# Optimization experiments

Hardware: AMD Instinct MI355X
Metric: run time of the kernel (lower is better)

Reference implementation:

```python
import jax, jax.numpy as jnp
import numpy as np

B, C, H, W = 8, 512, 32, 32
N_HEADS, HEAD_DIM = 8, 64
EPS = 1e-5


def _layernorm(x, g, b):
    mu = jnp.mean(x, axis=-1, keepdims=True)
    var = jnp.mean(jnp.square(x - mu), axis=-1, keepdims=True)
    return (x - mu) * jax.lax.rsqrt(var + EPS) * g + b


def setup_inputs() -> dict:
    key = jax.random.key(0)
    ks = jax.random.split(key, 16)
    u = lambda k, shp: jax.random.uniform(k, shp, dtype=jnp.float32)
    inp = {
        "x": jax.random.normal(ks[0], (B, C, H, W), dtype=jnp.float32),
        "t": jax.random.normal(ks[1], (B,), dtype=jnp.float32),
        # attention params (torch.rand init in source)
        "K_W": u(ks[2], (N_HEADS, C, HEAD_DIM)), "K_b": u(ks[3], (N_HEADS, HEAD_DIM)),
        "Q_W": u(ks[4], (N_HEADS, C, HEAD_DIM)), "Q_b": u(ks[5], (N_HEADS, HEAD_DIM)),
        "V_W": u(ks[6], (N_HEADS, C, HEAD_DIM)), "V_b": u(ks[7], (N_HEADS, HEAD_DIM)),
        "O_W": u(ks[8], (N_HEADS, HEAD_DIM, C)), "O_b": u(ks[9], (C,)),
        # pre-attention LayerNorm
        "ln1_g": jnp.ones((C,), jnp.float32), "ln1_b": jnp.zeros((C,), jnp.float32),
        # MLP: LayerNorm -> Linear -> GELU -> Linear
        "ln2_g": jnp.ones((C,), jnp.float32), "ln2_b": jnp.zeros((C,), jnp.float32),
        "W1": jax.random.normal(ks[10], (C, C), dtype=jnp.float32) / np.sqrt(C),
        "b1": jnp.zeros((C,), jnp.float32),
        "W2": jax.random.normal(ks[11], (C, C), dtype=jnp.float32) / np.sqrt(C),
        "b2": jnp.zeros((C,), jnp.float32),
    }
    return inp


def reference(x, t, K_W, K_b, Q_W, Q_b, V_W, V_b, O_W, O_b,
              ln1_g, ln1_b, ln2_g, ln2_b, W1, b1, W2, b2):
    b, c, h, w = x.shape
    xs = x.reshape(b, c, h * w).transpose(0, 2, 1)           # b s c
    res = _layernorm(xs, ln1_g, ln1_b)
    q = jnp.einsum('bsc,ncd->bsnd', res, Q_W) + Q_b          # b s n_h h_dim
    k = jnp.einsum('bsc,ncd->bsnd', res, K_W) + K_b
    v = jnp.einsum('bsc,ncd->bsnd', res, V_W) + V_b
    scores = jnp.einsum('bsnd,btnd->bnst', q, k) / jnp.sqrt(jnp.float32(c))
    attn = jax.nn.softmax(scores, axis=-1)                   # b n_h s s
    o = jnp.einsum('bnst,btnd->bsnd', attn, v)
    out = jnp.einsum('bsnd,ndc->bsc', o, O_W) + O_b
    out = out + xs                                           # residual
    m = _layernorm(out, ln2_g, ln2_b)
    m = jax.nn.gelu(m @ W1 + b1, approximate=False) @ W2 + b2
    out = m + out
    return out.transpose(0, 2, 1).reshape(b, c, h, w)
```

## Files before the change

### kernel.cpp

```cpp
#include <hip/hip_runtime.h>
#include <math.h>

#define BB 8
#define CC 512
#define SS 1024
#define NHH 8
#define HDD 64
#define KD 512

typedef __attribute__((ext_vector_type(8))) short short8;
typedef __attribute__((ext_vector_type(4))) float f32x4;
typedef __attribute__((ext_vector_type(4))) unsigned short ushort4v;
typedef __attribute__((ext_vector_type(8))) unsigned short ushort8v;
typedef __attribute__((ext_vector_type(2))) unsigned int u32x2;

__device__ __forceinline__ unsigned short f2bf(float x) {
  union { float f; unsigned int u; } c; c.f = x;
  unsigned int r = (c.u + 0x7FFFu + ((c.u >> 16) & 1u)) >> 16;
  return (unsigned short)r;
}
__device__ __forceinline__ float b2f(unsigned short h) {
  union { unsigned int u; float f; } c; c.u = ((unsigned int)h) << 16; return c.f;
}

#define GLD_LDS(gp, lp) __builtin_amdgcn_global_load_lds( \
    (const __attribute__((address_space(1))) void*)(gp),  \
    (__attribute__((address_space(3))) void*)(lp), 16, 0, 0)

__device__ __forceinline__ float block_reduce_sum(float v) {
  __shared__ float sm[4];
  #pragma unroll
  for (int o = 32; o > 0; o >>= 1) v += __shfl_down(v, o, 64);
  if ((threadIdx.x & 63) == 0) sm[threadIdx.x >> 6] = v;
  __syncthreads();
  float r = (sm[0] + sm[1]) + (sm[2] + sm[3]);
  __syncthreads();
  return r;
}

__global__ __launch_bounds__(256) void ln1_apply(
    const float* __restrict__ x, const float2* __restrict__ mustd,
    const float* __restrict__ g, const float* __restrict__ be,
    unsigned short* __restrict__ yh, unsigned short* __restrict__ yl,
    float* __restrict__ xf) {
  __shared__ float tile[32][33];
  const int b = blockIdx.z, c0 = blockIdx.y * 32, s0 = blockIdx.x * 32;
  const int tx = threadIdx.x, ty = threadIdx.y;
  const float* xb = x + ((size_t)b * CC + c0) * SS + s0;
  #pragma unroll
  for (int i = ty; i < 32; i += 8)
    tile[i][tx] = xb[(size_t)i * SS + tx];
  __syncthreads();
  const float gc = g[c0 + tx], bc = be[c0 + tx];
  #pragma unroll
  for (int i = ty; i < 32; i += 8) {
    const float2 ms = mustd[b * SS + s0 + i];
    const float v = tile[tx][i];
    const float y = (v - ms.x) * ms.y * gc + bc;
    const size_t oi = ((size_t)b * SS + s0 + i) * CC + c0 + tx;
    const unsigned short hy = f2bf(y);
    yh[oi] = hy; yl[oi] = f2bf(y - b2f(hy));
    xf[oi] = v;
  }
}

__global__ __launch_bounds__(256) void ln_bf16_k(const float* __restrict__ in,
                                                 const float* __restrict__ g,
                                                 const float* __restrict__ be,
                                                 unsigned short* __restrict__ outh) {
  const int wv = threadIdx.x >> 6, ln = threadIdx.x & 63;
  const size_t row = (size_t)blockIdx.x * 4 + wv;
  const float* r = in + row * CC + ln * 8;
  const float4 v0 = *(const float4*)(r);
  const float4 v1 = *(const float4*)(r + 4);
  float s = (v0.x + v0.y + v0.z + v0.w) + (v1.x + v1.y + v1.z + v1.w);
  #pragma unroll
  for (int o = 32; o > 0; o >>= 1) s += __shfl_xor(s, o, 64);
  const float mu = s * (1.0f / CC);
  float d[8] = {v0.x - mu, v0.y - mu, v0.z - mu, v0.w - mu,
                v1.x - mu, v1.y - mu, v1.z - mu, v1.w - mu};
  float q = 0.f;
  #pragma unroll
  for (int i = 0; i < 8; ++i) q += d[i] * d[i];
  #pragma unroll
  for (int o = 32; o > 0; o >>= 1) q += __shfl_xor(q, o, 64);
  const float rstd = rsqrtf(q * (1.0f / CC) + 1e-5f);
  const float4 g0 = *(const float4*)(g + ln * 8);
  const float4 g1 = *(const float4*)(g + ln * 8 + 4);
  const float4 b0 = *(const float4*)(be + ln * 8);
  const float4 b1 = *(const float4*)(be + ln * 8 + 4);
  const float gv[8] = {g0.x, g0.y, g0.z, g0.w, g1.x, g1.y, g1.z, g1.w};
  const float bv[8] = {b0.x, b0.y, b0.z, b0.w, b1.x, b1.y, b1.z, b1.w};
  ushort8v o8;
  #pragma unroll
  for (int i = 0; i < 8; ++i) o8[i] = f2bf(d[i] * rstd * gv[i] + bv[i]);
  *(ushort8v*)(outh + row * CC + ln * 8) = o8;
}

__global__ __launch_bounds__(256) void convert_and_stats(
    const float* __restrict__ QW, const float* __restrict__ KW,
    const float* __restrict__ VW, const float* __restrict__ OW,
    const float* __restrict__ W1, const float* __restrict__ W2,
    const float* __restrict__ Qb, const float* __restrict__ Kb,
    const float* __restrict__ Vb,
    unsigned short* __restrict__ BtQKh, unsigned short* __restrict__ BtQKl,
    unsigned short* __restrict__ BtVh,
    unsigned short* __restrict__ BtOh, unsigned short* __restrict__ BtOl,
    unsigned short* __restrict__ BtW1h, unsigned short* __restrict__ BtW2h,
    float* __restrict__ qkvb,
    const float* __restrict__ x, float2* __restrict__ mustd) {
  const int bid = blockIdx.x;
  if (bid < 1536) {
    const float SCL = 0.044194173824159216f * 1.4426950408889634f;
    __shared__ float tile[32][33];
    const int bx = bid & 15, by = (bid >> 4) & 1, p = bid >> 5;
    const int wsel = p >> 3, sub = p & 7;
    const int k0 = bx * 32, d0 = by * 32;
    const int tx = threadIdx.x & 31, ty = threadIdx.x >> 5;
    const float* w; int rs; unsigned short *dh, *dl; int nbase; float mul = 1.0f;
    switch (wsel) {
      case 0:  w = QW + sub * 32768; rs = 64;  dh = BtQKh; dl = BtQKl;  nbase = sub * 64; mul = SCL; break;
      case 1:  w = KW + sub * 32768; rs = 64;  dh = BtQKh; dl = BtQKl;  nbase = 512 + sub * 64;  break;
      case 2:  w = VW + sub * 32768; rs = 64;  dh = BtVh;  dl = nullptr; nbase = sub * 64;       break;
      case 3:  w = OW + sub * 64;    rs = 512; dh = BtOh;  dl = BtOl;   nbase = sub * 64;        break;
      case 4:  w = W1 + sub * 64;    rs = 512; dh = BtW1h; dl = nullptr; nbase = sub * 64;       break;
      default: w = W2 + sub * 64;    rs = 512; dh = BtW2h; dl = nullptr; nbase = sub * 64;       break;
    }
    for (int i = ty; i < 32; i += 8)
      tile[i][tx] = w[(size_t)(k0 + i) * rs + d0 + tx];
    __syncthreads();
    for (int i = ty; i < 32; i += 8) {
      float f = tile[tx][i] * mul;
      unsigned short h = f2bf(f);
      size_t idx = (size_t)(nbase + d0 + i) * KD + k0 + tx;
      dh[idx] = h;
      if (dl) dl[idx] = f2bf(f - b2f(h));
    }
    if (bid == 0) {
      int t = threadIdx.x;
      for (int i = t; i < 1536; i += 256)
        qkvb[i] = i < 512 ? Qb[i] * SCL : (i < 1024 ? Kb[i - 512] : Vb[i - 1024]);
    }
  } else {
    const int bid2 = bid - 1536;
    const int b = bid2 >> 4, s0 = (bid2 & 15) * 64;
    const int sl = threadIdx.x & 63, cg = threadIdx.x >> 6;
    const float* xp = x + (size_t)b * CC * SS + s0 + sl;
    float ps = 0.f, pq = 0.f;
    #pragma unroll 8
    for (int i = 0; i < 128; ++i) {
      const float v = xp[(size_t)(cg * 128 + i) * SS];
      ps += v; pq += v * v;
    }
    __shared__ float sred[2][4][64];
    sred[0][cg][sl] = ps; sred[1][cg][sl] = pq;
    __syncthreads();
    if (cg == 0) {
      const float s = (sred[0][0][sl] + sred[0][1][sl]) + (sred[0][2][sl] + sred[0][3][sl]);
      const float q = (sred[1][0][sl] + sred[1][1][sl]) + (sred[1][2][sl] + sred[1][3][sl]);
      const float mu = s * (1.0f / CC);
      const float rs = rsqrtf(q * (1.0f / CC) - mu * mu + 1e-5f);
      mustd[b * SS + s0 + sl] = make_float2(mu, rs);
    }
  }
}

__global__ __launch_bounds__(256) void gemm_qkv(
    const unsigned short* __restrict__ Ah, const unsigned short* __restrict__ Al,
    const unsigned short* __restrict__ Bth, const unsigned short* __restrict__ Btl,
    const float* __restrict__ bias,
    unsigned short* __restrict__ qkh, unsigned short* __restrict__ qkl,
    unsigned short* __restrict__ vt) {
  __shared__ __align__(16) unsigned short smem[4 * 128 * 32];
  unsigned short* As = smem;
  unsigned short* Bs = smem + 2 * 128 * 32;
  const int tid = threadIdx.x;
  const int w = tid >> 6, l = tid & 63, quad = l >> 4, lm = l & 15;
  const int f = blockIdx.x, xcd = f & 7, gidx = f >> 3;
  const int n0 = (gidx >> 3) * 128;
  const int m0 = (((gidx & 7) << 3) | xcd) * 128;
  const bool splitB = n0 < 1024;
  const int wm = (w >> 1) * 64, wn = (w & 1) * 64;
  const int srow = tid >> 2;
  const int sch = (((tid & 3) ^ (srow & 3)) * 8);
  const unsigned short* Agh = Ah + (size_t)(m0 + srow) * KD + sch;
  const unsigned short* Agl = Al + (size_t)(m0 + srow) * KD + sch;
  const unsigned short* Bgh = Bth + (size_t)(n0 + srow) * KD + sch;
  const unsigned short* Bgl = Btl + (size_t)(n0 + srow) * KD + sch;
  unsigned short* Aswh = As + w * 512;
  unsigned short* Aswl = As + 4096 + w * 512;
  unsigned short* Bswh = Bs + w * 512;
  unsigned short* Bswl = Bs + 4096 + w * 512;
  const int rch = ((quad ^ (lm & 3)) * 8);
  const f32x4 fzero = {0.f, 0.f, 0.f, 0.f};
  f32x4 acc[4][4];
  #pragma unroll
  for (int i = 0; i < 4; ++i)
    #pragma unroll
    for (int j = 0; j < 4; ++j) acc[i][j] = fzero;
  for (int k0 = 0; k0 < KD; k0 += 32) {
    __syncthreads();
    GLD_LDS(Agh + k0, Aswh);
    GLD_LDS(Agh + k0 + 64 * KD, Aswh + 2048);
    GLD_LDS(Agl + k0, Aswl);
    GLD_LDS(Agl + k0 + 64 * KD, Aswl + 2048);
    GLD_LDS(Bgh + k0, Bswh);
    GLD_LDS(Bgh + k0 + 64 * KD, Bswh + 2048);
    if (splitB) {
      GLD_LDS(Bgl + k0, Bswl);
      GLD_LDS(Bgl + k0 + 64 * KD, Bswl + 2048);
    }
    __syncthreads();
    short8 afh[4], afl[4], bfh[4], bfl[4];
    #pragma unroll
    for (int i = 0; i < 4; ++i) {
      afh[i] = *(const short8*)(As + (wm + i * 16 + lm) * 32 + rch);
      afl[i] = *(const short8*)(As + 4096 + (wm + i * 16 + lm) * 32 + rch);
    }
    #pragma unroll
    for (int j = 0; j < 4; ++j)
      bfh[j] = *(const short8*)(Bs + (wn + j * 16 + lm) * 32 + rch);
    if (splitB) {
      #pragma unroll
      for (int j = 0; j < 4; ++j)
        bfl[j] = *(const short8*)(Bs + 4096 + (wn + j * 16 + lm) * 32 + rch);
      #pragma unroll
      for (int i = 0; i < 4; ++i)
        #pragma unroll
        for (int j = 0; j < 4; ++j) {
          f32x4 t = acc[i][j];
          t = __builtin_amdgcn_mfma_f32_16x16x32_bf16(afh[i], bfh[j], t, 0, 0, 0);
          t = __builtin_amdgcn_mfma_f32_16x16x32_bf16(afh[i], bfl[j], t, 0, 0, 0);
          t = __builtin_amdgcn_mfma_f32_16x16x32_bf16(afl[i], bfh[j], t, 0, 0, 0);
          acc[i][j] = t;
        }
    } else {
      #pragma unroll
      for (int i = 0; i < 4; ++i)
        #pragma unroll
        for (int j = 0; j < 4; ++j)
          acc[i][j] = __builtin_amdgcn_mfma_f32_16x16x32_bf16(afh[i], bfh[j], acc[i][j], 0, 0, 0);
    }
  }
  if (splitB) {
    #pragma unroll
    for (int i = 0; i < 4; ++i) {
      const int row = m0 + wm + i * 16 + quad * 4;
      #pragma unroll
      for (int j = 0; j < 4; ++j) {
        const int ncol = n0 + wn + j * 16 + lm;
        const float bv = bias[ncol];
        #pragma unroll
        for (int r = 0; r < 4; ++r) {
          const float xv = acc[i][j][r] + bv;
          const size_t oi = (size_t)(row + r) * 1024 + ncol;
          unsigned short h = f2bf(xv);
          qkh[oi] = h;
          qkl[oi] = f2bf(xv - b2f(h));
        }
      }
    }
  } else {
    __syncthreads();
    #pragma unroll
    for (int i = 0; i < 4; ++i) {
      const int mlb = wm + i * 16 + quad * 4;
      #pragma unroll
      for (int j = 0; j < 4; ++j) {
        const int nl = wn + j * 16 + lm;
        const float bv = bias[n0 + nl];
        ushort4v pk;
        #pragma unroll
        for (int r = 0; r < 4; ++r) pk[r] = f2bf(acc[i][j][r] + bv);
        const int chunk = ((mlb >> 3) ^ (nl & 15));
        *(ushort4v*)(smem + nl * 128 + chunk * 8 + (mlb & 7)) = pk;
      }
    }
    __syncthreads();
    const int tn = tid >> 4, tc = tid & 15;
    const int bb2 = m0 >> 10, sbase = m0 & 1023;
    #pragma unroll
    for (int pass = 0; pass < 8; ++pass) {
      const int nl = pass * 16 + tn;
      const int hh = (n0 - 1024 + nl) >> 6, dd = nl & 63;
      short8 v8 = *(const short8*)(smem + nl * 128 + ((tc ^ (nl & 15)) * 8));
      *(short8*)(vt + ((size_t)(bb2 * 8 + hh) * 64 + dd) * 1024 + sbase + tc * 8) = v8;
    }
  }
}

template<int SB, int GELU, int OUTMODE, int RESID, int TRANS>
__global__ __launch_bounds__(256) void gemm64(
    const unsigned short* __restrict__ Ah,
    const unsigned short* __restrict__ Bh, const unsigned short* __restrict__ Bl,
    const float* __restrict__ bias, const float* __restrict__ residf,
    const unsigned short* __restrict__ residh, const unsigned short* __restrict__ residl,
    unsigned short* __restrict__ outh, float* __restrict__ outf, int ldc) {
  constexpr int STAGE = (SB ? 3 : 2) * 8192;
  constexpr int TSIZE = TRANS ? 64 * 65 * 4 : 0;
  __shared__ __align__(16) unsigned char smem[STAGE > TSIZE ? STAGE : TSIZE];
  unsigned short* As  = (unsigned short*)smem;
  unsigned short* Bs  = (unsigned short*)(smem + 8192);
  unsigned short* Bls = (unsigned short*)(smem + 16384);
  float (*ttile)[65]  = (float(*)[65])smem;
  const int tid = threadIdx.x;
  const int w = tid >> 6, l = tid & 63, quad = l >> 4, lm = l & 15;
  const int f = blockIdx.x, xcd = f & 7, gidx = f >> 3;
  const int n0 = (gidx >> 4) * 64;
  const int m0 = (((gidx & 15) << 3) | xcd) * 64;
  const int wm = (w >> 1) * 32, wn = (w & 1) * 32;
  const int srow8 = tid >> 3;
  const int sch8  = ((tid & 7) ^ (srow8 & 7)) * 8;
  const unsigned short* Ag  = Ah + (size_t)(m0 + srow8) * KD + sch8;
  const unsigned short* Bg  = Bh + (size_t)(n0 + srow8) * KD + sch8;
  const unsigned short* Bgl = SB ? Bl + (size_t)(n0 + srow8) * KD + sch8 : nullptr;
  const f32x4 fzero = {0.f, 0.f, 0.f, 0.f};
  f32x4 acc[2][2];
  #pragma unroll
  for (int i = 0; i < 2; ++i)
    #pragma unroll
    for (int j = 0; j < 2; ++j) acc[i][j] = fzero;
  for (int k0 = 0; k0 < KD; k0 += 64) {
    __syncthreads();
    GLD_LDS(Ag + k0, As + w * 512);
    GLD_LDS(Ag + k0 + 32 * KD, As + 2048 + w * 512);
    GLD_LDS(Bg + k0, Bs + w * 512);
    GLD_LDS(Bg + k0 + 32 * KD, Bs + 2048 + w * 512);
    if constexpr (SB) {
      GLD_LDS(Bgl + k0, Bls + w * 512);
      GLD_LDS(Bgl + k0 + 32 * KD, Bls + 2048 + w * 512);
    }
    __syncthreads();
    #pragma unroll
    for (int ks = 0; ks < 2; ++ks) {
      const int kc = ((ks * 4 + quad) ^ (lm & 7)) * 8;
      short8 af[2], bfh[2], bfl[2];
      #pragma unroll
      for (int i = 0; i < 2; ++i)
        af[i] = *(const short8*)(As + (wm + i * 16 + lm) * 64 + kc);
      #pragma unroll
      for (int j = 0; j < 2; ++j)
        bfh[j] = *(const short8*)(Bs + (wn + j * 16 + lm) * 64 + kc);
      if constexpr (SB) {
        #pragma unroll
        for (int j = 0; j < 2; ++j)
          bfl[j] = *(const short8*)(Bls + (wn + j * 16 + lm) * 64 + kc);
      }
      #pragma unroll
      for (int i = 0; i < 2; ++i)
        #pragma unroll
        for (int j = 0; j < 2; ++j) {
          f32x4 t = acc[i][j];
          t = __builtin_amdgcn_mfma_f32_16x16x32_bf16(af[i], bfh[j], t, 0, 0, 0);
          if constexpr (SB)
            t = __builtin_amdgcn_mfma_f32_16x16x32_bf16(af[i], bfl[j], t, 0, 0, 0);
          acc[i][j] = t;
        }
    }
  }
  if constexpr (TRANS) __syncthreads();
  #pragma unroll
  for (int i = 0; i < 2; ++i) {
    const int row = m0 + wm + i * 16 + quad * 4;
    #pragma unroll
    for (int j = 0; j < 2; ++j) {
      const int col = n0 + wn + j * 16 + lm;
      const float bv = bias[col];
      #pragma unroll
      for (int r = 0; r < 4; ++r) {
        float x = acc[i][j][r] + bv;
        if (GELU) x = 0.5f * x * (1.0f + erff(x * 0.70710678118654752f));
        const size_t ri = (size_t)(row + r) * CC + col;
        if (RESID == 1) x += residf[ri];
        if (RESID == 2) x += b2f(residh[ri]) + b2f(residl[ri]);
        if constexpr (TRANS) {
          ttile[wm + i * 16 + quad * 4 + r][wn + j * 16 + lm] = x;
        } else {
          const size_t oi = (size_t)(row + r) * ldc + col;
          if (OUTMODE == 0) outf[oi] = x;
          else outh[oi] = f2bf(x);
        }
      }
    }
  }
  if constexpr (TRANS) {
    __syncthreads();
    const int bi = m0 >> 10, s0 = m0 & 1023;
    const int s = tid & 63;
    #pragma unroll
    for (int c0 = 0; c0 < 64; c0 += 4) {
      const int col = c0 + (tid >> 6);
      outf[(size_t)(bi * 512 + n0 + col) * 1024 + s0 + s] = ttile[s][col];
    }
  }
}

__global__ __launch_bounds__(256) void attn_mfma(
    const unsigned short* __restrict__ QKh, const unsigned short* __restrict__ QKl,
    const unsigned short* __restrict__ Vt, unsigned short* __restrict__ Oh) {
  __shared__ __align__(16) unsigned short Ksh[64 * 64], Ksl[64 * 64];
  __shared__ __align__(16) unsigned short Vts[64 * 64];
  __shared__ __align__(16) unsigned short Pts[4][16 * 64];
  const int f = blockIdx.x, xcd = f & 7, gidx = f >> 3;
  const int bh = (xcd << 3) | (gidx >> 4);
  const int q0 = (gidx & 15) * 64, h = bh & 7, b = bh >> 3;
  const int tid = threadIdx.x, w = tid >> 6, l = tid & 63, quad = l >> 4, lm = l & 15;
  const int LDQ = 2 * CC;
  const size_t qkbase = (size_t)b * SS * LDQ;
  const int srow8 = tid >> 3;
  const int sch8  = ((tid & 7) ^ (srow8 & 7)) * 8;
  const unsigned short* Vg  = Vt + ((size_t)(b * 8 + h) * 64 + srow8) * 1024 + sch8;
  const unsigned short* kgh = QKh + qkbase + (size_t)srow8 * LDQ + CC + h * 64 + sch8;
  const unsigned short* kgl = QKl + qkbase + (size_t)srow8 * LDQ + CC + h * 64 + sch8;
  const int lofs = w * 512 + l * 8;
  short8 qh[2], ql[2];
  {
    const size_t qo = qkbase + (size_t)(q0 + w * 16 + lm) * LDQ + h * 64 + quad * 8;
    qh[0] = *(const short8*)(QKh + qo);
    qh[1] = *(const short8*)(QKh + qo + 32);
    ql[0] = *(const short8*)(QKl + qo);
    ql[1] = *(const short8*)(QKl + qo + 32);
  }
  const f32x4 fzero = {0.f, 0.f, 0.f, 0.f};
  float m = -1e30f, lsum = 0.f;
  f32x4 oacc[4];
  #pragma unroll
  for (int j = 0; j < 4; ++j) oacc[j] = fzero;
  unsigned char* Pb = (unsigned char*)(Pts[w]);
  const int pwbase = lm * 128 + ((quad & 1) << 3);
  const int prbase = lm * 128;
  short8 s0h = *(const short8*)(kgh);
  short8 s1h = *(const short8*)(kgh + (size_t)32 * LDQ);
  short8 s0l = *(const short8*)(kgl);
  short8 s1l = *(const short8*)(kgl + (size_t)32 * LDQ);
  short8 s0v = *(const short8*)(Vg);
  short8 s1v = *(const short8*)(Vg + 32 * 1024);
  for (int kt = 0; kt < SS; kt += 64) {
    __syncthreads();
    *(short8*)(Ksh + lofs)        = s0h;
    *(short8*)(Ksh + 2048 + lofs) = s1h;
    *(short8*)(Ksl + lofs)        = s0l;
    *(short8*)(Ksl + 2048 + lofs) = s1l;
    *(short8*)(Vts + lofs)        = s0v;
    *(short8*)(Vts + 2048 + lofs) = s1v;
    __syncthreads();
    {
      const int ktn = (kt + 64) & (SS - 1);
      s0h = *(const short8*)(kgh + (size_t)ktn * LDQ);
      s1h = *(const short8*)(kgh + (size_t)(ktn + 32) * LDQ);
      s0l = *(const short8*)(kgl + (size_t)ktn * LDQ);
      s1l = *(const short8*)(kgl + (size_t)(ktn + 32) * LDQ);
      s0v = *(const short8*)(Vg + ktn);
      s1v = *(const short8*)(Vg + ktn + 32 * 1024);
    }
    f32x4 sc[4];
    __builtin_amdgcn_s_setprio(1);
    {
      const int kc = (quad ^ (lm & 7)) * 8;
      #pragma unroll
      for (int j = 0; j < 4; ++j) {
        short8 kh = *(const short8*)(Ksh + (j * 16 + lm) * 64 + kc);
        short8 kl = *(const short8*)(Ksl + (j * 16 + lm) * 64 + kc);
        f32x4 t = __builtin_amdgcn_mfma_f32_16x16x32_bf16(kh, qh[0], fzero, 0, 0, 0);
        t = __builtin_amdgcn_mfma_f32_16x16x32_bf16(kl, qh[0], t, 0, 0, 0);
        t = __builtin_amdgcn_mfma_f32_16x16x32_bf16(kh, ql[0], t, 0, 0, 0);
        sc[j] = t;
      }
    }
    {
      const int kc = ((4 + quad) ^ (lm & 7)) * 8;
      #pragma unroll
      for (int j = 0; j < 4; ++j) {
        short8 kh = *(const short8*)(Ksh + (j * 16 + lm) * 64 + kc);
        short8 kl = *(const short8*)(Ksl + (j * 16 + lm) * 64 + kc);
        f32x4 t = sc[j];
        t = __builtin_amdgcn_mfma_f32_16x16x32_bf16(kh, qh[1], t, 0, 0, 0);
        t = __builtin_amdgcn_mfma_f32_16x16x32_bf16(kl, qh[1], t, 0, 0, 0);
        t = __builtin_amdgcn_mfma_f32_16x16x32_bf16(kh, ql[1], t, 0, 0, 0);
        sc[j] = t;
      }
    }
    __builtin_amdgcn_s_setprio(0);
    float mt0 = fmaxf(fmaxf(sc[0][0], sc[0][1]), fmaxf(sc[0][2], sc[0][3]));
    float mt1 = fmaxf(fmaxf(sc[1][0], sc[1][1]), fmaxf(sc[1][2], sc[1][3]));
    float mt2 = fmaxf(fmaxf(sc[2][0], sc[2][1]), fmaxf(sc[2][2], sc[2][3]));
    float mt3 = fmaxf(fmaxf(sc[3][0], sc[3][1]), fmaxf(sc[3][2], sc[3][3]));
    float mt = fmaxf(fmaxf(mt0, mt1), fmaxf(mt2, mt3));
    mt = fmaxf(mt, __shfl_xor(mt, 16, 64));
    mt = fmaxf(mt, __shfl_xor(mt, 32, 64));
    const float mnew = fmaxf(m, mt);
    if (__any(mnew > m)) {
      const float alpha = exp2f(m - mnew);
      m = mnew;
      lsum *= alpha;
      #pragma unroll
      for (int j = 0; j < 4; ++j)
        #pragma unroll
        for (int r = 0; r < 4; ++r) oacc[j][r] *= alpha;
    }
    float ls = 0.f;
    #pragma unroll
    for (int j = 0; j < 4; ++j)
      #pragma unroll
      for (int r = 0; r < 4; ++r) {
        sc[j][r] = exp2f(sc[j][r] - m);
        ls += sc[j][r];
      }
    ls += __shfl_xor(ls, 16, 64);
    ls += __shfl_xor(ls, 32, 64);
    lsum += ls;
    #pragma unroll
    for (int j = 0; j < 4; ++j) {
      union { float f; unsigned int u; } c0, c1, c2, c3;
      c0.f = sc[j][0]; c1.f = sc[j][1]; c2.f = sc[j][2]; c3.f = sc[j][3];
      u32x2 pk;
      pk[0] = __builtin_amdgcn_perm(c1.u, c0.u, 0x07060302u);
      pk[1] = __builtin_amdgcn_perm(c3.u, c2.u, 0x07060302u);
      const int slot = ((j << 1) | (quad >> 1)) ^ (lm & 7);
      *(u32x2*)(Pb + pwbase + (slot << 4)) = pk;
    }
    __builtin_amdgcn_s_setprio(1);
    #pragma unroll
    for (int st = 0; st < 2; ++st) {
      short8 pf = *(const short8*)(Pb + prbase + ((((st << 2) | quad) ^ (lm & 7)) << 4));
      const int kc = ((st * 4 + quad) ^ (lm & 7)) * 8;
      #pragma unroll
      for (int j = 0; j < 4; ++j) {
        short8 vv = *(const short8*)(Vts + (j * 16 + lm) * 64 + kc);
        oacc[j] = __builtin_amdgcn_mfma_f32_16x16x32_bf16(vv, pf, oacc[j], 0, 0, 0);
      }
    }
    __builtin_amdgcn_s_setprio(0);
  }
  const float inv = 1.f / lsum;
  const size_t obase =
      (size_t)b * SS * CC + (size_t)(q0 + w * 16 + lm) * CC + h * 64 + quad * 4;
  #pragma unroll
  for (int j = 0; j < 4; ++j) {
    ushort4v pk;
    #pragma unroll
    for (int r = 0; r < 4; ++r) pk[r] = f2bf(oacc[j][r] * inv);
    *(ushort4v*)(Oh + obase + j * 16) = pk;
  }
}

extern "C" void kernel_launch(void* const* d_in, const int* in_sizes, int n_in,
                              void* d_out, int out_size, void* d_ws, size_t ws_size,
                              hipStream_t stream) {
  const float* x    = (const float*)d_in[0];
  const float* K_W  = (const float*)d_in[2];
  const float* K_b  = (const float*)d_in[3];
  const float* Q_W  = (const float*)d_in[4];
  const float* Q_b  = (const float*)d_in[5];
  const float* V_W  = (const float*)d_in[6];
  const float* V_b  = (const float*)d_in[7];
  const float* O_W  = (const float*)d_in[8];
  const float* O_b  = (const float*)d_in[9];
  const float* ln1g = (const float*)d_in[10];
  const float* ln1b = (const float*)d_in[11];
  const float* ln2g = (const float*)d_in[12];
  const float* ln2b = (const float*)d_in[13];
  const float* W1   = (const float*)d_in[14];
  const float* b1   = (const float*)d_in[15];
  const float* W2   = (const float*)d_in[16];
  const float* b2   = (const float*)d_in[17];
  float* out = (float*)d_out;

  unsigned char* ws = (unsigned char*)d_ws;
  const size_t MB = 1u << 20;
  unsigned short* qkh   = (unsigned short*)(ws);
  unsigned short* qkl   = (unsigned short*)(ws + 16 * MB);
  unsigned short* vt    = (unsigned short*)(ws + 32 * MB);
  unsigned short* ln1h  = (unsigned short*)(ws + 40 * MB);
  unsigned short* ln1l  = (unsigned short*)(ws + 48 * MB);
  float* xsf            = (float*)(ws + 56 * MB);
  unsigned short* oh    = ln1h;
  float* out1           = (float*)(ws + 72 * MB);
  unsigned short* ln2h  = qkh;
  unsigned short* geluh = (unsigned short*)(ws + 8 * MB);
  unsigned short* BtAll = (unsigned short*)(ws + 88 * MB);
  unsigned short* BtQKh = BtAll;
  unsigned short* BtVh  = BtAll + 1024 * 512;
  unsigned short* BtQKl = BtVh + 512 * 512;
  unsigned short* BtOh  = BtQKl + 1024 * 512;
  unsigned short* BtOl  = BtOh + 512 * 512;
  unsigned short* BtW1h = BtOl + 512 * 512;
  unsigned short* BtW2h = BtW1h + 512 * 512;
  float* qkvb           = (float*)(BtW2h + 512 * 512);
  float2* mustd         = (float2*)(ws + 96 * MB);

  dim3 tb32(32, 8);
  convert_and_stats<<<1536 + 128, 256, 0, stream>>>(
      Q_W, K_W, V_W, O_W, W1, W2, Q_b, K_b, V_b,
      BtQKh, BtQKl, BtVh, BtOh, BtOl, BtW1h, BtW2h, qkvb, x, mustd);
  ln1_apply<<<dim3(SS / 32, CC / 32, BB), tb32, 0, stream>>>(
      x, mustd, ln1g, ln1b, ln1h, ln1l, xsf);
  gemm_qkv<<<768, 256, 0, stream>>>(
      ln1h, ln1l, BtAll, BtQKl, qkvb, qkh, qkl, vt);
  attn_mfma<<<1024, 256, 0, stream>>>(qkh, qkl, vt, oh);
  gemm64<1, 0, 0, 1, 0><<<1024, 256, 0, stream>>>(
      oh, BtOh, BtOl, O_b, xsf, nullptr, nullptr, nullptr, out1, CC);
  ln_bf16_k<<<BB * SS / 4, 256, 0, stream>>>(out1, ln2g, ln2b, ln2h);
  gemm64<0, 1, 1, 0, 0><<<1024, 256, 0, stream>>>(
      ln2h, BtW1h, nullptr, b1, nullptr, nullptr, nullptr, geluh, nullptr, CC);
  gemm64<0, 0, 0, 1, 1><<<1024, 256, 0, stream>>>(
      geluh, BtW2h, nullptr, b2, out1, nullptr, nullptr, nullptr, out, CC);
}
```

Measured before the change: 265.9 us.

## Process two query tiles per wave in attention to reuse K/V fragments

Each attention block now covers 128 queries instead of 64, with each wave handling two 16-row query tiles. The K and V fragments loaded from shared memory are reused across both tiles, and the grid is halved. This cuts shared-memory reads and global K/V reloads per query, at the cost of roughly doubled accumulator registers and fewer blocks (512) to fill the GPU.

```diff
diff --git a/kernel.cpp b/kernel.cpp
--- a/kernel.cpp
+++ b/kernel.cpp
@@ -400,10 +400,10 @@
     const unsigned short* __restrict__ Vt, unsigned short* __restrict__ Oh) {
   __shared__ __align__(16) unsigned short Ksh[64 * 64], Ksl[64 * 64];
   __shared__ __align__(16) unsigned short Vts[64 * 64];
-  __shared__ __align__(16) unsigned short Pts[4][16 * 64];
+  __shared__ __align__(16) unsigned short Pts[4][2][16 * 64];
   const int f = blockIdx.x, xcd = f & 7, gidx = f >> 3;
-  const int bh = (xcd << 3) | (gidx >> 4);
-  const int q0 = (gidx & 15) * 64, h = bh & 7, b = bh >> 3;
+  const int bh = (xcd << 3) | (gidx >> 3);
+  const int q0 = (gidx & 7) * 128, h = bh & 7, b = bh >> 3;
   const int tid = threadIdx.x, w = tid >> 6, l = tid & 63, quad = l >> 4, lm = l & 15;
   const int LDQ = 2 * CC;
   const size_t qkbase = (size_t)b * SS * LDQ;
@@ -413,20 +413,23 @@
   const unsigned short* kgh = QKh + qkbase + (size_t)srow8 * LDQ + CC + h * 64 + sch8;
   const unsigned short* kgl = QKl + qkbase + (size_t)srow8 * LDQ + CC + h * 64 + sch8;
   const int lofs = w * 512 + l * 8;
-  short8 qh[2], ql[2];
-  {
-    const size_t qo = qkbase + (size_t)(q0 + w * 16 + lm) * LDQ + h * 64 + quad * 8;
-    qh[0] = *(const short8*)(QKh + qo);
-    qh[1] = *(const short8*)(QKh + qo + 32);
-    ql[0] = *(const short8*)(QKl + qo);
-    ql[1] = *(const short8*)(QKl + qo + 32);
+  short8 qh[2][2], ql[2][2];
+  #pragma unroll
+  for (int qi = 0; qi < 2; ++qi) {
+    const size_t qo =
+        qkbase + (size_t)(q0 + w * 32 + qi * 16 + lm) * LDQ + h * 64 + quad * 8;
+    qh[qi][0] = *(const short8*)(QKh + qo);
+    qh[qi][1] = *(const short8*)(QKh + qo + 32);
+    ql[qi][0] = *(const short8*)(QKl + qo);
+    ql[qi][1] = *(const short8*)(QKl + qo + 32);
   }
   const f32x4 fzero = {0.f, 0.f, 0.f, 0.f};
-  float m = -1e30f, lsum = 0.f;
-  f32x4 oacc[4];
-  #pragma unroll
-  for (int j = 0; j < 4; ++j) oacc[j] = fzero;
-  unsigned char* Pb = (unsigned char*)(Pts[w]);
+  float m[2] = {-1e30f, -1e30f}, lsum[2] = {0.f, 0.f};
+  f32x4 oacc[2][4];
+  #pragma unroll
+  for (int qi = 0; qi < 2; ++qi)
+    #pragma unroll
+    for (int j = 0; j < 4; ++j) oacc[qi][j] = fzero;
   const int pwbase = lm * 128 + ((quad & 1) << 3);
   const int prbase = lm * 128;
   short8 s0h = *(const short8*)(kgh);
@@ -453,94 +456,120 @@
       s0v = *(const short8*)(Vg + ktn);
       s1v = *(const short8*)(Vg + ktn + 32 * 1024);
     }
-    f32x4 sc[4];
+    f32x4 sc[2][4];
     __builtin_amdgcn_s_setprio(1);
     {
       const int kc = (quad ^ (lm & 7)) * 8;
+      short8 kh[4], kl[4];
       #pragma unroll
       for (int j = 0; j < 4; ++j) {
-        short8 kh = *(const short8*)(Ksh + (j * 16 + lm) * 64 + kc);
-        short8 kl = *(const short8*)(Ksl + (j * 16 + lm) * 64 + kc);
-        f32x4 t = __builtin_amdgcn_mfma_f32_16x16x32_bf16(kh, qh[0], fzero, 0, 0, 0);
-        t = __builtin_amdgcn_mfma_f32_16x16x32_bf16(kl, qh[0], t, 0, 0, 0);
-        t = __builtin_amdgcn_mfma_f32_16x16x32_bf16(kh, ql[0], t, 0, 0, 0);
-        sc[j] = t;
-      }
+        kh[j] = *(const short8*)(Ksh + (j * 16 + lm) * 64 + kc);
+        kl[j] = *(const short8*)(Ksl + (j * 16 + lm) * 64 + kc);
+      }
+      #pragma unroll
+      for (int qi = 0; qi < 2; ++qi)
+        #pragma unroll
+        for (int j = 0; j < 4; ++j) {
+          f32x4 t = __builtin_amdgcn_mfma_f32_16x16x32_bf16(kh[j], qh[qi][0], fzero, 0, 0, 0);
+          t = __builtin_amdgcn_mfma_f32_16x16x32_bf16(kl[j], qh[qi][0], t, 0, 0, 0);
+          t = __builtin_amdgcn_mfma_f32_16x16x32_bf16(kh[j], ql[qi][0], t, 0, 0, 0);
+          sc[qi][j] = t;
+        }
     }
     {
       const int kc = ((4 + quad) ^ (lm & 7)) * 8;
+      short8 kh[4], kl[4];
       #pragma unroll
       for (int j = 0; j < 4; ++j) {
-        short8 kh = *(const short8*)(Ksh + (j * 16 + lm) * 64 + kc);
-        short8 kl = *(const short8*)(Ksl + (j * 16 + lm) * 64 + kc);
-        f32x4 t = sc[j];
-        t = __builtin_amdgcn_mfma_f32_16x16x32_bf16(kh, qh[1], t, 0, 0, 0);
-        t = __builtin_amdgcn_mfma_f32_16x16x32_bf16(kl, qh[1], t, 0, 0, 0);
-        t = __builtin_amdgcn_mfma_f32_16x16x32_bf16(kh, ql[1], t, 0, 0, 0);
-        sc[j] = t;
-      }
+        kh[j] = *(const short8*)(Ksh + (j * 16 + lm) * 64 + kc);
+        kl[j] = *(const short8*)(Ksl + (j * 16 + lm) * 64 + kc);
+      }
+      #pragma unroll
+      for (int qi = 0; qi < 2; ++qi)
+        #pragma unroll
+        for (int j = 0; j < 4; ++j) {
+          f32x4 t = sc[qi][j];
+          t = __builtin_amdgcn_mfma_f32_16x16x32_bf16(kh[j], qh[qi][1], t, 0, 0, 0);
+          t = __builtin_amdgcn_mfma_f32_16x16x32_bf16(kl[j], qh[qi][1], t, 0, 0, 0);
+          t = __builtin_amdgcn_mfma_f32_16x16x32_bf16(kh[j], ql[qi][1], t, 0, 0, 0);
+          sc[qi][j] = t;
+        }
     }
     __builtin_amdgcn_s_setprio(0);
-    float mt0 = fmaxf(fmaxf(sc[0][0], sc[0][1]), fmaxf(sc[0][2], sc[0][3]));
-    float mt1 = fmaxf(fmaxf(sc[1][0], sc[1][1]), fmaxf(sc[1][2], sc[1][3]));
-    float mt2 = fmaxf(fmaxf(sc[2][0], sc[2][1]), fmaxf(sc[2][2], sc[2][3]));
-    float mt3 = fmaxf(fmaxf(sc[3][0], sc[3][1]), fmaxf(sc[3][2], sc[3][3]));
-    float mt = fmaxf(fmaxf(mt0, mt1), fmaxf(mt2, mt3));
-    mt = fmaxf(mt, __shfl_xor(mt, 16, 64));
-    mt = fmaxf(mt, __shfl_xor(mt, 32, 64));
-    const float mnew = fmaxf(m, mt);
-    if (__any(mnew > m)) {
-      const float alpha = exp2f(m - mnew);
-      m = mnew;
-      lsum *= alpha;
+    #pragma unroll
+    for (int qi = 0; qi < 2; ++qi) {
+      float mt0 = fmaxf(fmaxf(sc[qi][0][0], sc[qi][0][1]), fmaxf(sc[qi][0][2], sc[qi][0][3]));
+      float mt1 = fmaxf(fmaxf(sc[qi][1][0], sc[qi][1][1]), fmaxf(sc[qi][1][2], sc[qi][1][3]));
+      float mt2 = fmaxf(fmaxf(sc[qi][2][0], sc[qi][2][1]), fmaxf(sc[qi][2][2], sc[qi][2][3]));
+      float mt3 = fmaxf(fmaxf(sc[qi][3][0], sc[qi][3][1]), fmaxf(sc[qi][3][2], sc[qi][3][3]));
+      float mt = fmaxf(fmaxf(mt0, mt1), fmaxf(mt2, mt3));
+      mt = fmaxf(mt, __shfl_xor(mt, 16, 64));
+      mt = fmaxf(mt, __shfl_xor(mt, 32, 64));
+      const float mnew = fmaxf(m[qi], mt);
+      if (__any(mnew > m[qi])) {
+        const float alpha = exp2f(m[qi] - mnew);
+        m[qi] = mnew;
+        lsum[qi] *= alpha;
+        #pragma unroll
+        for (int j = 0; j < 4; ++j)
+          #pragma unroll
+          for (int r = 0; r < 4; ++r) oacc[qi][j][r] *= alpha;
+      }
+      float ls = 0.f;
       #pragma unroll
       for (int j = 0; j < 4; ++j)
         #pragma unroll
-        for (int r = 0; r < 4; ++r) oacc[j][r] *= alpha;
-    }
-    float ls = 0.f;
-    #pragma unroll
-    for (int j = 0; j < 4; ++j)
-      #pragma unroll
-      for (int r = 0; r < 4; ++r) {
-        sc[j][r] = exp2f(sc[j][r] - m);
-        ls += sc[j][r];
-      }
-    ls += __shfl_xor(ls, 16, 64);
-    ls += __shfl_xor(ls, 32, 64);
-    lsum += ls;
+        for (int r = 0; r < 4; ++r) {
+          sc[qi][j][r] = exp2f(sc[qi][j][r] - m[qi]);
+          ls += sc[qi][j][r];
+        }
+      ls += __shfl_xor(ls, 16, 64);
+      ls += __shfl_xor(ls, 32, 64);
+      lsum[qi] += ls;
+      unsigned char* Pb = (unsigned char*)(Pts[w][qi]);
+      #pragma unroll
+      for (int j = 0; j < 4; ++j) {
+        union { float f; unsigned int u; } c0, c1, c2, c3;
+        c0.f = sc[qi][j][0]; c1.f = sc[qi][j][1];
+        c2.f = sc[qi][j][2]; c3.f = sc[qi][j][3];
+        u32x2 pk;
+        pk[0] = __builtin_amdgcn_perm(c1.u, c0.u, 0x07060302u);
+        pk[1] = __builtin_amdgcn_perm(c3.u, c2.u, 0x07060302u);
+        const int slot = ((j << 1) | (quad >> 1)) ^ (lm & 7);
+        *(u32x2*)(Pb + pwbase + (slot << 4)) = pk;
+      }
+    }
+    __builtin_amdgcn_s_setprio(1);
+    #pragma unroll
+    for (int st = 0; st < 2; ++st) {
+      const int kc = ((st * 4 + quad) ^ (lm & 7)) * 8;
+      short8 vv[4];
+      #pragma unroll
+      for (int j = 0; j < 4; ++j)
+        vv[j] = *(const short8*)(Vts + (j * 16 + lm) * 64 + kc);
+      #pragma unroll
+      for (int qi = 0; qi < 2; ++qi) {
+        short8 pf = *(const short8*)((unsigned char*)(Pts[w][qi]) + prbase +
+                                     ((((st << 2) | quad) ^ (lm & 7)) << 4));
+        #pragma unroll
+        for (int j = 0; j < 4; ++j)
+          oacc[qi][j] = __builtin_amdgcn_mfma_f32_16x16x32_bf16(vv[j], pf, oacc[qi][j], 0, 0, 0);
+      }
+    }
+    __builtin_amdgcn_s_setprio(0);
+  }
+  #pragma unroll
+  for (int qi = 0; qi < 2; ++qi) {
+    const float inv = 1.f / lsum[qi];
+    const size_t obase = (size_t)b * SS * CC +
+        (size_t)(q0 + w * 32 + qi * 16 + lm) * CC + h * 64 + quad * 4;
     #pragma unroll
     for (int j = 0; j < 4; ++j) {
-      union { float f; unsigned int u; } c0, c1, c2, c3;
-      c0.f = sc[j][0]; c1.f = sc[j][1]; c2.f = sc[j][2]; c3.f = sc[j][3];
-      u32x2 pk;
-      pk[0] = __builtin_amdgcn_perm(c1.u, c0.u, 0x07060302u);
-      pk[1] = __builtin_amdgcn_perm(c3.u, c2.u, 0x07060302u);
-      const int slot = ((j << 1) | (quad >> 1)) ^ (lm & 7);
-      *(u32x2*)(Pb + pwbase + (slot << 4)) = pk;
-    }
-    __builtin_amdgcn_s_setprio(1);
-    #pragma unroll
-    for (int st = 0; st < 2; ++st) {
-      short8 pf = *(const short8*)(Pb + prbase + ((((st << 2) | quad) ^ (lm & 7)) << 4));
-      const int kc = ((st * 4 + quad) ^ (lm & 7)) * 8;
-      #pragma unroll
-      for (int j = 0; j < 4; ++j) {
-        short8 vv = *(const short8*)(Vts + (j * 16 + lm) * 64 + kc);
-        oacc[j] = __builtin_amdgcn_mfma_f32_16x16x32_bf16(vv, pf, oacc[j], 0, 0, 0);
-      }
-    }
-    __builtin_amdgcn_s_setprio(0);
-  }
-  const float inv = 1.f / lsum;
-  const size_t obase =
-      (size_t)b * SS * CC + (size_t)(q0 + w * 16 + lm) * CC + h * 64 + quad * 4;
-  #pragma unroll
-  for (int j = 0; j < 4; ++j) {
-    ushort4v pk;
-    #pragma unroll
-    for (int r = 0; r < 4; ++r) pk[r] = f2bf(oacc[j][r] * inv);
-    *(ushort4v*)(Oh + obase + j * 16) = pk;
+      ushort4v pk;
+      #pragma unroll
+      for (int r = 0; r < 4; ++r) pk[r] = f2bf(oacc[qi][j][r] * inv);
+      *(ushort4v*)(Oh + obase + j * 16) = pk;
+    }
   }
 }
 
@@ -597,7 +626,7 @@
       x, mustd, ln1g, ln1b, ln1h, ln1l, xsf);
   gemm_qkv<<<768, 256, 0, stream>>>(
       ln1h, ln1l, BtAll, BtQKl, qkvb, qkh, qkl, vt);
-  attn_mfma<<<1024, 256, 0, stream>>>(qkh, qkl, vt, oh);
+  attn_mfma<<<512, 256, 0, stream>>>(qkh, qkl, vt, oh);
   gemm64<1, 0, 0, 1, 0><<<1024, 256, 0, stream>>>(
       oh, BtOh, BtOl, O_b, xsf, nullptr, nullptr, nullptr, out1, CC);
   ln_bf16_k<<<BB * SS / 4, 256, 0, stream>>>(out1, ln2g, ln2b, ln2h);
```

New measurement: 257.5 us. -3.2%, faster.
